# Kernel optimization log

Hardware: AMD Instinct MI355X
Metric: run time of the kernel (lower is better)

Reference implementation:

```python
import jax, jax.numpy as jnp
import numpy as np


def setup_inputs() -> dict:
    key = jax.random.key(0)
    ks = jax.random.split(key, 5)
    B, Cin, Cout, H, W, L, K = 16, 512, 512, 64, 64, 512, 3
    return {
        "content": jax.random.normal(ks[0], (B, Cin, H, W), jnp.float32),
        "latent": jax.random.normal(ks[1], (B, L), jnp.float32),
        "noise": jax.random.normal(ks[2], (B, 1, H, W), jnp.float32),
        "affine_w": jax.random.normal(ks[3], (Cin, L), jnp.float32),
        "affine_b": jnp.ones((Cin,), jnp.float32),  # ConvLayer fills affine bias with 1
        "conv_w": jax.random.normal(ks[4], (Cout, Cin, K, K), jnp.float32),
        "bias": jnp.zeros((1, Cout, 1, 1), jnp.float32),
        "noise_weight": jnp.asarray(0.1, jnp.float32),  # nonzero so noise path is exercised
    }


def reference(content, latent, noise, affine_w, affine_b, conv_w, bias, noise_weight):
    L = affine_w.shape[1]
    # affine (LinearLayer, lrelu=False): weight scaled by sqrt(1/inChannels), lrMultiplier=1
    style = latent @ (affine_w * np.sqrt(1.0 / L)).T + affine_b  # [B, Cin]
    # modulate: per-sample weights [B, Cout, Cin, k, k]
    w = conv_w[None] * style[:, None, :, None, None]
    # demodulate
    norm = jax.lax.rsqrt(jnp.sum(jnp.square(w), axis=(2, 3, 4), keepdims=True) + 1e-8)
    w = w * norm
    pad = conv_w.shape[-1] // 2
    # groups=batch trick == per-sample conv; vmap over batch
    def conv1(x, wk):  # x: [Cin,H,W], wk: [Cout,Cin,k,k]
        return jax.lax.conv_general_dilated(x[None], wk, (1, 1), [(pad, pad), (pad, pad)])[0]
    out = jax.vmap(conv1)(content, w)  # [B, Cout, H, W]
    out = out + noise_weight * noise
    out = jax.nn.leaky_relu(out + bias, negative_slope=0.2) * np.sqrt(2.0)
    return out
```

## Files before the change

### kernel.cpp

```cpp
#include <hip/hip_runtime.h>
#include <hip/hip_bf16.h>


typedef float f32x4 __attribute__((ext_vector_type(4)));
typedef float f32x16 __attribute__((ext_vector_type(16)));
typedef short bf16x8 __attribute__((ext_vector_type(8)));
typedef int i32x4 __attribute__((ext_vector_type(4)));

#define BB 16
#define CIN 512
#define COUT 512
#define HH 64
#define WW 64
#define LL 512

#define X3ROWB 2176
#define X3C16B (66 * X3ROWB)
#define X3BB (32 * X3C16B)
#define XS3_SZ (16 * X3BB)

#define WT3_STEPB 147456
#define WT3_SZ (32 * WT3_STEPB)

#define XS3_OFF 0
#define WT3_OFF XS3_SZ
#define STYLE_OFF (WT3_OFF + WT3_SZ)
#define STYLE_SZ (BB * CIN * 4)
#define WSQ_OFF (STYLE_OFF + STYLE_SZ)
#define WSQ_SZ (COUT * CIN * 4)
#define DEM_OFF (WSQ_OFF + WSQ_SZ)
#define DEM_SZ (BB * COUT * 4)
#define WS_NEEDED (DEM_OFF + DEM_SZ)

#define XSTEPB 22528
#define WSTEPB 18432

__device__ __forceinline__ void gld_lds16(const void* g, void* l) {
  __builtin_amdgcn_global_load_lds(
      (const __attribute__((address_space(1))) unsigned int*)g,
      (__attribute__((address_space(3))) unsigned int*)l, 16, 0, 0);
}

__global__ void style_kernel(const float* __restrict__ latent,
                             const float* __restrict__ affine_w,
                             const float* __restrict__ affine_b,
                             float* __restrict__ style) {
  const int idx = blockIdx.x * 256 + threadIdx.x;
  const int b = idx >> 9, ci = idx & 511;
  const float* lp = latent + b * LL;
  const float* wp = affine_w + ci * LL;
  float acc = 0.f;
  for (int l = 0; l < LL; ++l) acc += lp[l] * wp[l];
  style[idx] = acc * 0.044194173824159216f + affine_b[ci];
}

__global__ void wprep_kernel(const float* __restrict__ conv_w,
                             float* __restrict__ wsq,
                             __hip_bfloat16* __restrict__ wt3) {
  const int idx = blockIdx.x * 256 + threadIdx.x;
  const int co = idx >> 9, ci = idx & 511;
  const float* wp = conv_w + idx * 9;
  const int cib = ci >> 4, h = (ci >> 3) & 1, ci8 = ci & 7;
  __hip_bfloat16* base = wt3 + (size_t)cib * 73728 + h * 4096 + co * 8 + ci8;
  float ss = 0.f;
#pragma unroll
  for (int t = 0; t < 9; ++t) {
    float v = wp[t];
    ss += v * v;
    base[t * 8192] = __float2bfloat16(v);
  }
  wsq[idx] = ss;
}

__global__ void dem_kernel(const float* __restrict__ wsq,
                           const float* __restrict__ style,
                           float* __restrict__ dem) {
  const int idx = blockIdx.x * 256 + threadIdx.x;
  const int b = idx >> 9, co = idx & 511;
  const float* sp = style + b * CIN;
  const float* wp = wsq + co * CIN;
  float acc = 0.f;
  for (int ci = 0; ci < CIN; ++ci) {
    float s = sp[ci];
    acc += wp[ci] * s * s;
  }
  dem[idx] = 1.0f / sqrtf(acc + 1e-8f);
}

__global__ void xsprep_kernel(const float* __restrict__ content,
                              const float* __restrict__ style,
                              char* __restrict__ xs3) {
  __shared__ float tile[64][65];
  const int b = blockIdx.x >> 6;
  const int y = blockIdx.x & 63;
  const int tid = threadIdx.x;
  char* bbase = xs3 + (size_t)b * X3BB;

  {
    const int c16 = tid >> 3, rest = tid & 7;
    const int h = rest >> 2, pp = rest & 3;
    const int px = (pp == 0) ? 0 : 64 + pp;
    *(i32x4*)(bbase + (size_t)c16 * X3C16B + (y + 1) * X3ROWB + h * 1088 +
              px * 16) = (i32x4){0, 0, 0, 0};
  }
  if (y == 0 || y == 63) {
    const int rowidx = (y == 0) ? 0 : 65;
#pragma unroll
    for (int k = 0; k < 17; ++k) {
      const int u = tid + k * 256;
      if (u < 4352) {
        const int c16 = u / 136, w = u - c16 * 136;
        *(i32x4*)(bbase + (size_t)c16 * X3C16B + rowidx * X3ROWB + w * 16) =
            (i32x4){0, 0, 0, 0};
      }
    }
  }

  for (int cb = 0; cb < 8; ++cb) {
    const int ci0 = cb * 64;
    __syncthreads();
    {
      const int x = tid & 63;
      const int c0 = tid >> 6;
#pragma unroll
      for (int p = 0; p < 16; ++p) {
        const int ci = p * 4 + c0;
        tile[ci][x] = content[((b * CIN + ci0 + ci) * HH + y) * WW + x];
      }
    }
    __syncthreads();
    {
      const int x = tid & 63;
      const int o4 = tid >> 6;
#pragma unroll
      for (int oo = 0; oo < 2; ++oo) {
        const int oct = o4 * 2 + oo;
        const int c16 = cb * 4 + (oct >> 1);
        const int h = oct & 1;
        bf16x8 v;
#pragma unroll
        for (int j = 0; j < 8; ++j) {
          const float st = style[b * CIN + ci0 + oct * 8 + j];
          v[j] = __bfloat16_as_short(
              __float2bfloat16(tile[oct * 8 + j][x] * st));
        }
        *(bf16x8*)(bbase + (size_t)c16 * X3C16B + (y + 1) * X3ROWB + h * 1088 +
                   (x + 1) * 16) = v;
      }
    }
  }
}

__global__ __launch_bounds__(256, 2) void conv_kernel(
    const char* __restrict__ xs3,
    const char* __restrict__ wt3,
    const float* __restrict__ dem,
    const float* __restrict__ noise,
    const float* __restrict__ biasp,
    const float* __restrict__ nwp,
    float* __restrict__ out) {
  __shared__ __attribute__((aligned(16))) char xlds[2][XSTEPB];
  __shared__ __attribute__((aligned(16))) char wlds[2][WSTEPB];

  const int tid = threadIdx.x;
  const int lane = tid & 63;
  const int wv = tid >> 6;
  const int l31 = lane & 31;
  const int hsel = lane >> 5;

  const int d = blockIdx.x;
  const int L = (d & 7) * 128 + (d >> 3);
  const int cot = L & 7;
  const int yo = (L >> 3) & 7;
  const int b = L >> 6;
  const int co0 = cot << 6;
  const int y0 = yo << 3;

  const char* xsrc[6];
#pragma unroll
  for (int k = 0; k < 6; ++k) {
    const int c = wv + 4 * k;
    if (c < 22) {
      const int beta = c * 1024 + lane * 16;
      const int row = beta / X3ROWB;
      const int within = beta - row * X3ROWB;
      xsrc[k] = xs3 + (size_t)(b * 32) * X3C16B +
                (size_t)(y0 + row) * X3ROWB + within;
    } else {
      xsrc[k] = xs3;
    }
  }
  const char* wsrc[5];
#pragma unroll
  for (int k = 0; k < 5; ++k) {
    const int c = wv + 4 * k;
    if (c < 18) {
      const int tap = c >> 1, h = c & 1;
      wsrc[k] = wt3 + tap * 16384 + h * 8192 + (co0 + lane) * 16;
    } else {
      wsrc[k] = wt3;
    }
  }

  const int abase0 = hsel * 1024 + l31 * 16;
  const int bbase0 = hsel * 1088 + l31 * 16;
  const int xwrow = 2 * wv * X3ROWB;

  f32x16 acc[2][2][2];
#pragma unroll
  for (int mf = 0; mf < 2; ++mf)
#pragma unroll
    for (int r = 0; r < 2; ++r)
#pragma unroll
      for (int q = 0; q < 2; ++q)
#pragma unroll
        for (int e = 0; e < 16; ++e) acc[mf][r][q][e] = 0.f;

  auto stage = [&](int t, int bi) {
    char* xd = xlds[bi];
    char* wd = wlds[bi];
    const size_t xadv = (size_t)t * X3C16B;
    const size_t wadv = (size_t)t * WT3_STEPB;
#pragma unroll
    for (int k = 0; k < 6; ++k) {
      const int c = wv + 4 * k;
      if (c < 22) gld_lds16(xsrc[k] + xadv, xd + c * 1024);
    }
#pragma unroll
    for (int k = 0; k < 5; ++k) {
      const int c = wv + 4 * k;
      if (c < 18) gld_lds16(wsrc[k] + wadv, wd + c * 1024);
    }
  };

  stage(0, 0);
  __syncthreads();

  for (int t = 0; t < 32; ++t) {
    const int bi = t & 1;
    if (t < 31) stage(t + 1, bi ^ 1);
    const char* xb = xlds[bi];
    const char* wb = wlds[bi];
#pragma unroll
    for (int dx = 0; dx < 3; ++dx) {
      bf16x8 a[3][2];
#pragma unroll
      for (int dy = 0; dy < 3; ++dy)
#pragma unroll
        for (int mf = 0; mf < 2; ++mf)
          a[dy][mf] = *(const bf16x8*)(wb + (dy * 3 + dx) * 2048 + abase0 +
                                       mf * 512);
#pragma unroll
      for (int ir = 0; ir < 4; ++ir) {
        const char* rp = xb + xwrow + ir * X3ROWB;
        bf16x8 bq[2];
#pragma unroll
        for (int q = 0; q < 2; ++q)
          bq[q] = *(const bf16x8*)(rp + bbase0 + (q * 32 + dx) * 16);
#pragma unroll
        for (int dy = 0; dy < 3; ++dy) {
          const int r = ir - dy;
          if (r == 0 || r == 1) {
#pragma unroll
            for (int q = 0; q < 2; ++q)
#pragma unroll
              for (int mf = 0; mf < 2; ++mf)
                acc[mf][r][q] = __builtin_amdgcn_mfma_f32_32x32x16_bf16(
                    a[dy][mf], bq[q], acc[mf][r][q], 0, 0, 0);
          }
        }
      }
    }
    __syncthreads();
  }

  const float nwv = nwp[0];
  float nz[2][2];
#pragma unroll
  for (int r = 0; r < 2; ++r) {
    const int y = y0 + 2 * wv + r;
#pragma unroll
    for (int q = 0; q < 2; ++q)
      nz[r][q] = nwv * noise[(b << 12) + (y << 6) + q * 32 + l31];
  }
#pragma unroll
  for (int mf = 0; mf < 2; ++mf)
#pragma unroll
    for (int reg = 0; reg < 16; ++reg) {
      const int coo = (reg & 3) + 8 * (reg >> 2) + 4 * hsel;
      const int co = co0 + mf * 32 + coo;
      const float dv = dem[(b << 9) + co];
      const float bv = biasp[co];
#pragma unroll
      for (int r = 0; r < 2; ++r) {
        const int y = y0 + 2 * wv + r;
#pragma unroll
        for (int q = 0; q < 2; ++q) {
          float v = acc[mf][r][q][reg] * dv + nz[r][q] + bv;
          v = (v > 0.f ? v : 0.2f * v) * 1.41421356237309515f;
          out[(((size_t)(b << 9) + co) << 12) + (y << 6) + q * 32 + l31] = v;
        }
      }
    }
}

extern "C" void kernel_launch(void* const* d_in, const int* in_sizes, int n_in,
                              void* d_out, int out_size, void* d_ws, size_t ws_size,
                              hipStream_t stream) {
  const float* content  = (const float*)d_in[0];
  const float* latent   = (const float*)d_in[1];
  const float* noise    = (const float*)d_in[2];
  const float* affine_w = (const float*)d_in[3];
  const float* affine_b = (const float*)d_in[4];
  const float* conv_w   = (const float*)d_in[5];
  const float* bias     = (const float*)d_in[6];
  const float* nw       = (const float*)d_in[7];
  float* out = (float*)d_out;
  char* ws = (char*)d_ws;

  if (ws_size < (size_t)WS_NEEDED) return;

  char* xs3 = ws + XS3_OFF;
  __hip_bfloat16* wt3 = (__hip_bfloat16*)(ws + WT3_OFF);
  float* style = (float*)(ws + STYLE_OFF);
  float* wsq   = (float*)(ws + WSQ_OFF);
  float* dem   = (float*)(ws + DEM_OFF);

  style_kernel<<<dim3(32), dim3(256), 0, stream>>>(latent, affine_w, affine_b, style);
  wprep_kernel<<<dim3(1024), dim3(256), 0, stream>>>(conv_w, wsq, wt3);
  dem_kernel<<<dim3(32), dim3(256), 0, stream>>>(wsq, style, dem);
  xsprep_kernel<<<dim3(1024), dim3(256), 0, stream>>>(content, style, xs3);
  conv_kernel<<<dim3(1024), dim3(256), 0, stream>>>(
      xs3, (const char*)(ws + WT3_OFF), dem, noise, bias, nw, out);
}
```

Before: 322.3 us.

## Split K-step into three barrier-phased stages interleaving global-to-LDS loads with MFMA

```diff
diff --git a/kernel.cpp b/kernel.cpp
--- a/kernel.cpp
+++ b/kernel.cpp
@@ -216,63 +216,71 @@
 #pragma unroll
         for (int e = 0; e < 16; ++e) acc[mf][r][q][e] = 0.f;
 
-  auto stage = [&](int t, int bi) {
-    char* xd = xlds[bi];
-    char* wd = wlds[bi];
-    const size_t xadv = (size_t)t * X3C16B;
-    const size_t wadv = (size_t)t * WT3_STEPB;
-#pragma unroll
-    for (int k = 0; k < 6; ++k) {
-      const int c = wv + 4 * k;
-      if (c < 22) gld_lds16(xsrc[k] + xadv, xd + c * 1024);
-    }
-#pragma unroll
-    for (int k = 0; k < 5; ++k) {
-      const int c = wv + 4 * k;
-      if (c < 18) gld_lds16(wsrc[k] + wadv, wd + c * 1024);
-    }
-  };
-
-  stage(0, 0);
-  __syncthreads();
+#define STG_X(K)                                                        \
+  if ((K) < 5 || wv < 2)                                                \
+    gld_lds16(xsrc[K] + xadv, xd + (wv + 4 * (K)) * 1024);
+#define STG_W(K)                                                        \
+  if ((K) < 4 || wv < 2)                                                \
+    gld_lds16(wsrc[K] + wadv, wd + (wv + 4 * (K)) * 1024);
+
+  {
+    char* xd = xlds[0];
+    char* wd = wlds[0];
+    const size_t xadv = 0, wadv = 0;
+    STG_X(0) STG_X(1) STG_X(2) STG_X(3) STG_X(4) STG_X(5)
+    STG_W(0) STG_W(1) STG_W(2) STG_W(3) STG_W(4)
+  }
+  asm volatile("s_waitcnt vmcnt(0)" ::: "memory");
+  __builtin_amdgcn_s_barrier();
+
+#define PHASE(DX, STGPART, TAIL)                                          \
+  {                                                                       \
+    bf16x8 aP[3][2], bP[4][2];                                            \
+    _Pragma("unroll") for (int dy = 0; dy < 3; ++dy)                      \
+        _Pragma("unroll") for (int mf = 0; mf < 2; ++mf)                  \
+            aP[dy][mf] = *(const bf16x8*)(wb + (dy * 3 + (DX)) * 2048 +   \
+                                          abase0 + mf * 512);             \
+    _Pragma("unroll") for (int ir = 0; ir < 4; ++ir)                      \
+        _Pragma("unroll") for (int q = 0; q < 2; ++q)                     \
+            bP[ir][q] = *(const bf16x8*)(xb + xwrow + ir * X3ROWB +       \
+                                         bbase0 + (q * 32 + (DX)) * 16);  \
+    if (t < 31) { STGPART }                                               \
+    __builtin_amdgcn_s_barrier();                                         \
+    asm volatile("s_waitcnt lgkmcnt(0)" ::: "memory");                    \
+    __builtin_amdgcn_sched_barrier(0);                                    \
+    __builtin_amdgcn_s_setprio(1);                                        \
+    _Pragma("unroll") for (int ir = 0; ir < 4; ++ir)                      \
+        _Pragma("unroll") for (int dy = 0; dy < 3; ++dy) {                \
+      const int rr = ir - dy;                                             \
+      if (rr == 0 || rr == 1) {                                           \
+        _Pragma("unroll") for (int q = 0; q < 2; ++q)                     \
+            _Pragma("unroll") for (int mf = 0; mf < 2; ++mf)              \
+                acc[mf][rr][q] = __builtin_amdgcn_mfma_f32_32x32x16_bf16( \
+                    aP[dy][mf], bP[ir][q], acc[mf][rr][q], 0, 0, 0);      \
+      }                                                                   \
+    }                                                                     \
+    __builtin_amdgcn_s_setprio(0);                                        \
+    TAIL;                                                                 \
+    __builtin_amdgcn_s_barrier();                                         \
+  }
 
   for (int t = 0; t < 32; ++t) {
     const int bi = t & 1;
-    if (t < 31) stage(t + 1, bi ^ 1);
     const char* xb = xlds[bi];
     const char* wb = wlds[bi];
-#pragma unroll
-    for (int dx = 0; dx < 3; ++dx) {
-      bf16x8 a[3][2];
-#pragma unroll
-      for (int dy = 0; dy < 3; ++dy)
-#pragma unroll
-        for (int mf = 0; mf < 2; ++mf)
-          a[dy][mf] = *(const bf16x8*)(wb + (dy * 3 + dx) * 2048 + abase0 +
-                                       mf * 512);
-#pragma unroll
-      for (int ir = 0; ir < 4; ++ir) {
-        const char* rp = xb + xwrow + ir * X3ROWB;
-        bf16x8 bq[2];
-#pragma unroll
-        for (int q = 0; q < 2; ++q)
-          bq[q] = *(const bf16x8*)(rp + bbase0 + (q * 32 + dx) * 16);
-#pragma unroll
-        for (int dy = 0; dy < 3; ++dy) {
-          const int r = ir - dy;
-          if (r == 0 || r == 1) {
-#pragma unroll
-            for (int q = 0; q < 2; ++q)
-#pragma unroll
-              for (int mf = 0; mf < 2; ++mf)
-                acc[mf][r][q] = __builtin_amdgcn_mfma_f32_32x32x16_bf16(
-                    a[dy][mf], bq[q], acc[mf][r][q], 0, 0, 0);
-          }
-        }
-      }
-    }
-    __syncthreads();
-  }
+    char* xd = xlds[bi ^ 1];
+    char* wd = wlds[bi ^ 1];
+    const size_t xadv = (size_t)(t + 1) * X3C16B;
+    const size_t wadv = (size_t)(t + 1) * WT3_STEPB;
+
+    PHASE(0, STG_X(0) STG_X(1) STG_W(0) STG_W(1), )
+    PHASE(1, STG_X(2) STG_X(3) STG_W(2) STG_W(3), )
+    PHASE(2, STG_X(4) STG_X(5) STG_W(4),
+          asm volatile("s_waitcnt vmcnt(0)" ::: "memory"))
+  }
+#undef PHASE
+#undef STG_X
+#undef STG_W
 
   const float nwv = nwp[0];
   float nz[2][2];
```

New measurement: 316.6 us. No clear change (-1.8%).
